# Optimization experiments

Measured on AMD Instinct MI355X. Metric: run time of the kernel, lower is better.

Reference implementation:

```python
import jax, jax.numpy as jnp
import numpy as np

N = 8192      # atoms
B = 64        # molecules
E = 262144    # edges
S = 4         # species
NMAX = 8      # radial basis size
CUT = 5.0     # cutoff radius
AVG_ATOMS = 128.0
E_SCALE = 1.0
PS_DIM = (S * NMAX) ** 2 * 4  # l_max=3 -> 4 l channels -> 4096
H1, H2 = 1024, 1024
OUT = 1


def _sph_harm(u):
    # real spherical harmonics up to l=3, input unit vectors [E,3] -> [E,16]
    x, y, z = u[:, 0], u[:, 1], u[:, 2]
    x2, y2, z2 = x * x, y * y, z * z
    return jnp.stack([
        0.28209479 * jnp.ones_like(x),
        0.48860251 * y, 0.48860251 * z, 0.48860251 * x,
        1.09254843 * x * y, 1.09254843 * y * z, 0.31539157 * (3.0 * z2 - 1.0),
        1.09254843 * x * z, 0.54627422 * (x2 - y2),
        0.59004359 * y * (3.0 * x2 - y2), 2.89061144 * x * y * z,
        0.45704579 * y * (5.0 * z2 - 1.0), 0.37317633 * z * (5.0 * z2 - 3.0),
        0.45704579 * x * (5.0 * z2 - 1.0), 1.44530572 * z * (x2 - y2),
        0.59004359 * x * (x2 - 3.0 * y2),
    ], axis=-1)


def setup_inputs() -> dict:
    key = jax.random.key(0)
    ks = jax.random.split(key, 12)
    positions = jax.random.normal(ks[0], (N, 3), dtype=jnp.float32) * 1.5  # dense cloud so many pairs < CUT
    cells = jnp.tile(20.0 * jnp.eye(3, dtype=jnp.float32)[None], (B, 1, 1))
    numbers = jax.random.randint(ks[1], (N,), 0, S)
    edge_indices = jax.random.randint(ks[2], (2, E), 0, N)
    edge_offsets = jnp.zeros((E, 3), dtype=jnp.float32)
    batch = jnp.arange(N) // (N // B)
    gamma = 1.0 + 0.1 * jax.random.normal(ks[3], (PS_DIM,), dtype=jnp.float32)
    beta = 0.1 * jax.random.normal(ks[4], (PS_DIM,), dtype=jnp.float32)
    W_ps = jax.random.normal(ks[5], (PS_DIM, OUT), dtype=jnp.float32) / np.sqrt(PS_DIM)
    W1 = jax.random.normal(ks[6], (PS_DIM, H1), dtype=jnp.float32) / np.sqrt(PS_DIM)
    W2 = jax.random.normal(ks[7], (H1, H2), dtype=jnp.float32) / np.sqrt(H1)
    W3 = jax.random.normal(ks[8], (H2, OUT), dtype=jnp.float32) / np.sqrt(H2)
    W_comp = jax.random.normal(ks[9], (S, OUT), dtype=jnp.float32) / np.sqrt(S)
    return dict(positions=positions, cells=cells, numbers=numbers,
                edge_indices=edge_indices, edge_offsets=edge_offsets, batch=batch,
                gamma=gamma, beta=beta, W_ps=W_ps, W1=W1, W2=W2, W3=W3, W_comp=W_comp)


def reference(positions, cells, numbers, edge_indices, edge_offsets, batch,
              gamma, beta, W_ps, W1, W2, W3, W_comp):
    i, j = edge_indices[0], edge_indices[1]  # center, neighbor
    # periodic shift: fractional offsets through the cell of the center's molecule
    shift = jnp.einsum('ec,ecd->ed', edge_offsets, cells[batch[i]])
    rvec = positions[j] - positions[i] + shift                      # [E,3]
    r = jnp.sqrt(jnp.sum(rvec * rvec, axis=-1) + 1e-12)             # [E]
    u = rvec / r[:, None]
    fc = 0.5 * (jnp.cos(jnp.pi * jnp.minimum(r, CUT) / CUT) + 1.0) * (r < CUT)
    n = jnp.arange(1, NMAX + 1, dtype=positions.dtype)
    R = fc[:, None] * jnp.sin(jnp.pi * n[None, :] * r[:, None] / CUT) / r[:, None]  # [E,NMAX]
    Y = _sph_harm(u)                                                # [E,16]
    edge_feat = R[:, :, None] * Y[:, None, :]                       # [E,NMAX,16]
    # spherical expansion c[i, species(j), n, lm] via scatter-add
    seg = i * S + numbers[j]
    c = jax.ops.segment_sum(edge_feat, seg, num_segments=N * S)     # [N*S,NMAX,16]
    c = c.reshape(N, S * NMAX, 16)
    # power spectrum: contract over m within each l block
    bounds = [(0, 1), (1, 4), (4, 9), (9, 16)]
    p = [jnp.einsum('ixm,iym->ixy', c[:, :, s:e], c[:, :, s:e]) for s, e in bounds]
    ps = jnp.stack(p, axis=-1).reshape(N, PS_DIM)                   # [N,4096]
    # LayerNorm (eps=1e-5, affine)
    mu = jnp.mean(ps, axis=-1, keepdims=True)
    var = jnp.var(ps, axis=-1, keepdims=True)
    psn = (ps - mu) / jnp.sqrt(var + 1e-5) * gamma + beta
    # linear branch + MLP branch
    psl = psn @ W_ps                                                # [N,1]
    h = jax.nn.silu(psn @ W1)
    h = jax.nn.silu(h @ W2)
    psnn = h @ W3                                                   # [N,1]
    # pool atomic energies into per-molecule totals (index_add)
    energies = jax.ops.segment_sum(psl + psnn, batch, num_segments=B) / AVG_ATOMS
    # eval path: composition baseline
    comp = jax.ops.segment_sum(jax.nn.one_hot(numbers, S, dtype=psn.dtype), batch, num_segments=B)
    return energies * E_SCALE + comp @ W_comp                       # [B,1]
```

## Files before the change

kernel.cpp:

```cpp
#include <hip/hip_runtime.h>
#include <hip/hip_bf16.h>
#include <math.h>

#define N_ATOMS 8192
#define B_BATCH 64
#define E_EDGES 262144
#define S_SPEC 4
#define NMAX 8
#define PS_DIM 4096
#define H1_DIM 1024
#define CAP4 48
#define CUTR 5.0f
#define PI_F 3.14159265358979f

typedef __bf16 bf16;
typedef bf16 bf16x8 __attribute__((ext_vector_type(8)));
typedef float floatx4 __attribute__((ext_vector_type(4)));
typedef int intx8 __attribute__((ext_vector_type(8)));
typedef unsigned char u8;

__device__ __forceinline__ void g2lds16(const void* g, void* l) {
    __builtin_amdgcn_global_load_lds(
        (const __attribute__((address_space(1))) void*)g,
        (__attribute__((address_space(3))) void*)l, 16, 0, 0);
}

__device__ __forceinline__ int pk_fp8x4(float a, float b, float c, float d) {
    int lo = __builtin_amdgcn_cvt_pk_fp8_f32(a, b, 0, false);
    return __builtin_amdgcn_cvt_pk_fp8_f32(c, d, lo, true);
}

__global__ __launch_bounds__(256) void scatter_kernel(
    const float* __restrict__ pos, const float* __restrict__ cells,
    const int* __restrict__ numbers, const int* __restrict__ ei,
    const float* __restrict__ eo, const int* __restrict__ batch,
    int* __restrict__ cnt, float4* __restrict__ bucket)
{
    int e = blockIdx.x * 256 + threadIdx.x;
    int i = ei[e];
    int j = ei[E_EDGES + e];
    int b = batch[i];
    const float* cell = cells + b * 9;
    float o0 = eo[e * 3 + 0], o1 = eo[e * 3 + 1], o2 = eo[e * 3 + 2];
    float rv[3];
    #pragma unroll
    for (int d = 0; d < 3; ++d) {
        float shift = o0 * cell[0 * 3 + d] + o1 * cell[1 * 3 + d] + o2 * cell[2 * 3 + d];
        rv[d] = pos[j * 3 + d] - pos[i * 3 + d] + shift;
    }
    float r2 = rv[0] * rv[0] + rv[1] * rv[1] + rv[2] * rv[2] + 1e-12f;
    if (r2 >= CUTR * CUTR) return;
    float r = sqrtf(r2);
    float a1 = r * (PI_F / CUTR);
    int sp = numbers[j];
    int q = i * S_SPEC + sp;
    int slot = atomicAdd(&cnt[q], 1);
    if (slot < CAP4)
        bucket[q * CAP4 + slot] = make_float4(rv[0], rv[1], rv[2], a1);
}

__global__ __launch_bounds__(256) void accum_ps_kernel(
    const float4* __restrict__ bucket, const int* __restrict__ cnt,
    const float* __restrict__ gamma, const float* __restrict__ beta,
    const float* __restrict__ Wps, u8* __restrict__ psn, float* __restrict__ psl)
{
    __shared__ __align__(16) float cl[4][32 * 20];
    __shared__ __align__(16) u8 ps_s8[PS_DIM];
    __shared__ float red[8];
    __shared__ float red2[4];

    int t = threadIdx.x;
    int wv = t >> 6, lane = t & 63;
    int atom0 = blockIdx.x * 4;

    {
        int atom = atom0 + wv;
        int sp_l = lane >> 4;
        int nidx = (lane >> 1) & 7;
        float nf = (float)(nidx + 1);
        int par = lane & 1;

        int myCnt = cnt[atom * S_SPEC + sp_l];
        if (myCnt > CAP4) myCnt = CAP4;
        int m1 = max(myCnt, __shfl_xor(myCnt, 16));
        int mx = max(m1, __shfl_xor(m1, 32));

        const float4* q = bucket + (size_t)(atom * S_SPEC + sp_l) * CAP4;
        float acc[8] = {};
        #pragma unroll 2
        for (int e = 0; e < mx; ++e) {
            float4 d = q[e];
            bool valid = e < myCnt;
            float a1 = d.w;
            float inv_r = (PI_F / CUTR) * __frcp_rn(a1);
            float fc = 0.5f * __cosf(a1) + 0.5f;
            float rn = fc * inv_r * __sinf(nf * a1);
            rn = valid ? rn : 0.0f;

            float x = d.x * inv_r, y = d.y * inv_r, z = d.z * inv_r;
            float x2 = x * x, y2 = y * y, z2 = z * z;
            float Ys[8];
            if (par == 0) {
                Ys[0] = 0.28209479f;
                Ys[1] = 0.48860251f * y;
                Ys[2] = 0.48860251f * z;
                Ys[3] = 0.48860251f * x;
                Ys[4] = 1.09254843f * x * y;
                Ys[5] = 1.09254843f * y * z;
                Ys[6] = 0.31539157f * (3.0f * z2 - 1.0f);
                Ys[7] = 1.09254843f * x * z;
            } else {
                Ys[0] = 0.54627422f * (x2 - y2);
                Ys[1] = 0.59004359f * y * (3.0f * x2 - y2);
                Ys[2] = 2.89061144f * x * y * z;
                Ys[3] = 0.45704579f * y * (5.0f * z2 - 1.0f);
                Ys[4] = 0.37317633f * z * (5.0f * z2 - 3.0f);
                Ys[5] = 0.45704579f * x * (5.0f * z2 - 1.0f);
                Ys[6] = 1.44530572f * z * (x2 - y2);
                Ys[7] = 0.59004359f * x * (x2 - 3.0f * y2);
            }
            #pragma unroll
            for (int k = 0; k < 8; ++k) acc[k] += rn * Ys[k];
        }
        int X = sp_l * 8 + nidx;
        float* dst = &cl[wv][X * 20 + par * 8];
        *(float4*)(dst + 0) = make_float4(acc[0], acc[1], acc[2], acc[3]);
        *(float4*)(dst + 4) = make_float4(acc[4], acc[5], acc[6], acc[7]);
    }
    __syncthreads();

    for (int a = 0; a < 4; ++a) {
        int atom = atom0 + a;
        const float* cl_x = cl[a];

        int y = t & 31;
        int xb = t >> 5;
        float4 cya = *(const float4*)&cl_x[y * 20 + 0];
        float4 cyb = *(const float4*)&cl_x[y * 20 + 4];
        float4 cyc = *(const float4*)&cl_x[y * 20 + 8];
        float4 cyd = *(const float4*)&cl_x[y * 20 + 12];

        float ps[4][4];
        float sum = 0.0f, sumsq = 0.0f;
        #pragma unroll
        for (int q = 0; q < 4; ++q) {
            int x = xb + 8 * q;
            float4 xa = *(const float4*)&cl_x[x * 20 + 0];
            float4 xbv = *(const float4*)&cl_x[x * 20 + 4];
            float4 xc = *(const float4*)&cl_x[x * 20 + 8];
            float4 xd = *(const float4*)&cl_x[x * 20 + 12];
            float s0 = xa.x * cya.x;
            float s1 = xa.y * cya.y + xa.z * cya.z + xa.w * cya.w;
            float s2 = xbv.x * cyb.x + xbv.y * cyb.y + xbv.z * cyb.z + xbv.w * cyb.w
                     + xc.x * cyc.x;
            float s3 = xc.y * cyc.y + xc.z * cyc.z + xc.w * cyc.w
                     + xd.x * cyd.x + xd.y * cyd.y + xd.z * cyd.z + xd.w * cyd.w;
            ps[q][0] = s0; ps[q][1] = s1; ps[q][2] = s2; ps[q][3] = s3;
            sum += s0 + s1 + s2 + s3;
            sumsq += s0 * s0 + s1 * s1 + s2 * s2 + s3 * s3;
        }
        #pragma unroll
        for (int o = 32; o > 0; o >>= 1) {
            sum += __shfl_down(sum, o);
            sumsq += __shfl_down(sumsq, o);
        }
        if ((t & 63) == 0) { red[wv] = sum; red[4 + wv] = sumsq; }
        __syncthreads();
        float tot = red[0] + red[1] + red[2] + red[3];
        float totsq = red[4] + red[5] + red[6] + red[7];
        float mu = tot * (1.0f / PS_DIM);
        float var = totsq * (1.0f / PS_DIM) - mu * mu;
        float inv = rsqrtf(var + 1e-5f);

        float pacc = 0.0f;
        #pragma unroll
        for (int q = 0; q < 4; ++q) {
            int p = t + 256 * q;
            float4 g = *(const float4*)(gamma + p * 4);
            float4 bt = *(const float4*)(beta + p * 4);
            float4 w = *(const float4*)(Wps + p * 4);
            float v0 = (ps[q][0] - mu) * inv * g.x + bt.x;
            float v1 = (ps[q][1] - mu) * inv * g.y + bt.y;
            float v2 = (ps[q][2] - mu) * inv * g.z + bt.z;
            float v3 = (ps[q][3] - mu) * inv * g.w + bt.w;
            pacc += v0 * w.x + v1 * w.y + v2 * w.z + v3 * w.w;
            ((int*)ps_s8)[p] = pk_fp8x4(v0, v1, v2, v3);
        }
        __syncthreads();
        u8* rowp = psn + (size_t)atom * PS_DIM;
        int key = atom & 7;
        int gcs = (t & ~7) | ((t & 7) ^ key);
        *(uint4*)(rowp + (size_t)gcs * 16) = *(const uint4*)(ps_s8 + (size_t)t * 16);

        #pragma unroll
        for (int o = 32; o > 0; o >>= 1) pacc += __shfl_down(pacc, o);
        if ((t & 63) == 0) red2[wv] = pacc;
        __syncthreads();
        if (t == 0) psl[atom] = red2[0] + red2[1] + red2[2] + red2[3];
    }
}

__global__ __launch_bounds__(256) void transpose_convert2(
    const float* __restrict__ W1, u8* __restrict__ Wt1,
    const float* __restrict__ W2, u8* __restrict__ Wt2)
{
    const float* W; u8* Wt; int K; float scale; int bx;
    if (blockIdx.x < 128) { W = W1; Wt = Wt1; K = PS_DIM; scale = 64.0f; bx = blockIdx.x; }
    else                  { W = W2; Wt = Wt2; K = H1_DIM; scale = 32.0f; bx = blockIdx.x - 128; }
    const int Nc = H1_DIM;
    __shared__ float t[32][33];
    int k0 = bx * 32, n0 = blockIdx.y * 32;
    int tx = threadIdx.x & 31, ty = threadIdx.x >> 5;
    #pragma unroll
    for (int r = 0; r < 32; r += 8)
        t[ty + r][tx] = W[(size_t)(k0 + ty + r) * Nc + n0 + tx];
    __syncthreads();
    if (threadIdx.x < 64) {
        int nl = threadIdx.x >> 1, cc = threadIdx.x & 1;
        int n = n0 + nl;
        unsigned int w[4];
        #pragma unroll
        for (int g = 0; g < 4; ++g) {
            int kb = cc * 16 + g * 4;
            w[g] = (unsigned int)pk_fp8x4(
                t[kb + 0][nl] * scale, t[kb + 1][nl] * scale,
                t[kb + 2][nl] * scale, t[kb + 3][nl] * scale);
        }
        int gc = (k0 >> 4) + cc;
        int gcs = (gc & ~7) | ((gc & 7) ^ (n & 7));
        *(uint4*)(Wt + (size_t)n * K + (size_t)gcs * 16) = make_uint4(w[0], w[1], w[2], w[3]);
    }
}

template<int OUT_FP8>
__global__ __launch_bounds__(256) void gemm_f8_kernel(
    const u8* __restrict__ A, const u8* __restrict__ Bt,
    void* __restrict__ H, int M, int Nc, int K, float invs)
{
    __shared__ __align__(16) char smem[24576];
    int tid = threadIdx.x;
    int bm = blockIdx.x, bn = blockIdx.y;
    int wave = tid >> 6, lane = tid & 63;
    int wm = (wave >> 1) * 32, wn = (wave & 1) * 64;
    int lm = lane & 15, quad = lane >> 4;

    floatx4 acc[2][4] = {};
    const int rowA0 = bm * 64, rowB0 = bn * 128;
    const size_t stride = (size_t)K;
    const char* Ab = (const char*)A + (size_t)rowA0 * stride;
    const char* Bb = (const char*)Bt + (size_t)rowB0 * stride;
    const int sA = 0x7F7F7F7F, sB = 0x7F7F7F7F;

    for (int k0 = 0; k0 < K; k0 += 128) {
        #pragma unroll
        for (int s = 0; s < 2; ++s) {
            int L = s * 256 + tid;
            int row = L >> 3, boff = (L & 7) * 16;
            int lbase = (s * 256 + wave * 64) * 16;
            g2lds16(Ab + (size_t)row * stride + k0 + boff, smem + lbase);
        }
        #pragma unroll
        for (int s = 0; s < 4; ++s) {
            int L = s * 256 + tid;
            int row = L >> 3, boff = (L & 7) * 16;
            int lbase = (s * 256 + wave * 64) * 16;
            g2lds16(Bb + (size_t)row * stride + k0 + boff, smem + 8192 + lbase);
        }
        __syncthreads();
        int key = lm & 7;
        int c0 = (2 * quad) ^ key, c1 = (2 * quad + 1) ^ key;
        intx8 af[2], bfr[4];
        #pragma unroll
        for (int mi = 0; mi < 2; ++mi) {
            const char* base = smem + (wm + mi * 16 + lm) * 128;
            uint4 lo = *(const uint4*)(base + c0 * 16);
            uint4 hi = *(const uint4*)(base + c1 * 16);
            af[mi][0] = lo.x; af[mi][1] = lo.y; af[mi][2] = lo.z; af[mi][3] = lo.w;
            af[mi][4] = hi.x; af[mi][5] = hi.y; af[mi][6] = hi.z; af[mi][7] = hi.w;
        }
        #pragma unroll
        for (int ni = 0; ni < 4; ++ni) {
            const char* base = smem + 8192 + (wn + ni * 16 + lm) * 128;
            uint4 lo = *(const uint4*)(base + c0 * 16);
            uint4 hi = *(const uint4*)(base + c1 * 16);
            bfr[ni][0] = lo.x; bfr[ni][1] = lo.y; bfr[ni][2] = lo.z; bfr[ni][3] = lo.w;
            bfr[ni][4] = hi.x; bfr[ni][5] = hi.y; bfr[ni][6] = hi.z; bfr[ni][7] = hi.w;
        }
        #pragma unroll
        for (int mi = 0; mi < 2; ++mi)
            #pragma unroll
            for (int ni = 0; ni < 4; ++ni)
                acc[mi][ni] = __builtin_amdgcn_mfma_scale_f32_16x16x128_f8f6f4(
                    af[mi], bfr[ni], acc[mi][ni], 0, 0, 0, sA, 0, sB);
        __syncthreads();
    }

    if (OUT_FP8) {
        u8* Cs8 = (u8*)smem;
        #pragma unroll
        for (int mi = 0; mi < 2; ++mi)
            #pragma unroll
            for (int ni = 0; ni < 4; ++ni)
                #pragma unroll
                for (int r = 0; r < 4; ++r) {
                    int row = wm + mi * 16 + quad * 4 + r;
                    int col = wn + ni * 16 + lm;
                    float v = acc[mi][ni][r] * invs;
                    v = v / (1.0f + __expf(-v));
                    int pk = __builtin_amdgcn_cvt_pk_fp8_f32(v, 0.0f, 0, false);
                    Cs8[row * 128 + col] = (u8)(pk & 0xFF);
                }
        __syncthreads();
        #pragma unroll
        for (int c2 = 0; c2 < 2; ++c2) {
            int L = c2 * 256 + tid;
            int row = L >> 3, cc = L & 7;
            int gcs = cc ^ (row & 7);
            *(uint4*)((u8*)H + (size_t)(rowA0 + row) * Nc + (size_t)(bn * 8 + gcs) * 16) =
                *(const uint4*)(Cs8 + (size_t)L * 16);
        }
    } else {
        bf16* Cs = (bf16*)smem;
        #pragma unroll
        for (int mi = 0; mi < 2; ++mi)
            #pragma unroll
            for (int ni = 0; ni < 4; ++ni)
                #pragma unroll
                for (int r = 0; r < 4; ++r) {
                    int row = wm + mi * 16 + quad * 4 + r;
                    int col = wn + ni * 16 + lm;
                    float v = acc[mi][ni][r] * invs;
                    v = v / (1.0f + __expf(-v));
                    Cs[row * 128 + col] = (bf16)v;
                }
        __syncthreads();
        const size_t strideH = (size_t)Nc * 2;
        #pragma unroll
        for (int c2 = 0; c2 < 4; ++c2) {
            int L = c2 * 256 + tid;
            int row = L >> 4, cc = L & 15;
            *(uint4*)((char*)H + (size_t)(rowA0 + row) * strideH + (size_t)(bn * 16 + cc) * 16) =
                *(const uint4*)((char*)Cs + (size_t)L * 16);
        }
    }
}

__global__ __launch_bounds__(256) void tail_kernel(
    const bf16* __restrict__ h2, const float* __restrict__ W3,
    const float* __restrict__ psl, const int* __restrict__ numbers,
    const float* __restrict__ Wcomp, float* __restrict__ out)
{
    int b = blockIdx.x;
    int t = threadIdx.x;
    int wv = t >> 6, lane = t & 63;
    __shared__ float tot;
    __shared__ int cnt4[S_SPEC];
    if (t == 0) tot = 0.0f;
    if (t < S_SPEC) cnt4[t] = 0;
    __syncthreads();

    if (t < 128) {
        int a = b * 128 + t;
        atomicAdd(&tot, psl[a]);
        atomicAdd(&cnt4[numbers[a]], 1);
    }

    float acc = 0.0f;
    for (int k = 0; k < 32; ++k) {
        int atom = b * 128 + wv * 32 + k;
        const bf16* h = h2 + (size_t)atom * H1_DIM;
        #pragma unroll
        for (int q2 = 0; q2 < 2; ++q2) {
            int k0 = (lane + 64 * q2) * 8;
            bf16x8 hv = *(const bf16x8*)(h + k0);
            float4 w0 = *(const float4*)(W3 + k0);
            float4 w1 = *(const float4*)(W3 + k0 + 4);
            acc += (float)hv[0] * w0.x + (float)hv[1] * w0.y
                 + (float)hv[2] * w0.z + (float)hv[3] * w0.w
                 + (float)hv[4] * w1.x + (float)hv[5] * w1.y
                 + (float)hv[6] * w1.z + (float)hv[7] * w1.w;
        }
    }
    #pragma unroll
    for (int o = 32; o > 0; o >>= 1) acc += __shfl_down(acc, o);
    if (lane == 0) atomicAdd(&tot, acc);
    __syncthreads();
    if (t == 0) {
        float r = tot * (1.0f / 128.0f);
        #pragma unroll
        for (int s = 0; s < S_SPEC; ++s) r += (float)cnt4[s] * Wcomp[s];
        out[b] = r;
    }
}

extern "C" void kernel_launch(void* const* d_in, const int* in_sizes, int n_in,
                              void* d_out, int out_size, void* d_ws, size_t ws_size,
                              hipStream_t stream)
{
    const float* positions = (const float*)d_in[0];
    const float* cells     = (const float*)d_in[1];
    const int*   numbers   = (const int*)d_in[2];
    const int*   ei        = (const int*)d_in[3];
    const float* eo        = (const float*)d_in[4];
    const int*   batch     = (const int*)d_in[5];
    const float* gamma     = (const float*)d_in[6];
    const float* beta      = (const float*)d_in[7];
    const float* W_ps      = (const float*)d_in[8];
    const float* W1        = (const float*)d_in[9];
    const float* W2        = (const float*)d_in[10];
    const float* W3        = (const float*)d_in[11];
    const float* W_comp    = (const float*)d_in[12];
    float* out = (float*)d_out;

    char* ws = (char*)d_ws;
    float4* bucket = (float4*)ws;  ws += (size_t)N_ATOMS * S_SPEC * CAP4 * 16;
    u8*    psn  = (u8*)ws;     ws += (size_t)N_ATOMS * PS_DIM;
    u8*    h1   = (u8*)ws;     ws += (size_t)N_ATOMS * H1_DIM;
    bf16*  h2   = (bf16*)ws;   ws += (size_t)N_ATOMS * H1_DIM * 2;
    u8*    Wt1  = (u8*)ws;     ws += (size_t)H1_DIM * PS_DIM;
    u8*    Wt2  = (u8*)ws;     ws += (size_t)H1_DIM * H1_DIM;
    float* psl  = (float*)ws;  ws += (size_t)N_ATOMS * 4;
    int*   cnt  = (int*)ws;    ws += (size_t)N_ATOMS * S_SPEC * 4;

    hipMemsetAsync(cnt, 0, N_ATOMS * S_SPEC * sizeof(int), stream);

    scatter_kernel<<<E_EDGES / 256, 256, 0, stream>>>(
        positions, cells, numbers, ei, eo, batch, cnt, bucket);

    transpose_convert2<<<dim3(160, 32), 256, 0, stream>>>(W1, Wt1, W2, Wt2);

    accum_ps_kernel<<<N_ATOMS / 4, 256, 0, stream>>>(
        bucket, cnt, gamma, beta, W_ps, psn, psl);

    gemm_f8_kernel<1><<<dim3(N_ATOMS / 64, H1_DIM / 128), 256, 0, stream>>>(
        psn, Wt1, (void*)h1, N_ATOMS, H1_DIM, PS_DIM, 1.0f / 64.0f);
    gemm_f8_kernel<0><<<dim3(N_ATOMS / 64, H1_DIM / 128), 256, 0, stream>>>(
        h1, Wt2, (void*)h2, N_ATOMS, H1_DIM, H1_DIM, 1.0f / 32.0f);

    tail_kernel<<<B_BATCH, 256, 0, stream>>>(h2, W3, psl, numbers, W_comp, out);
}
```

Before: 214.0 us.

## Fuse W3 projection into second GEMM epilogue and merge scatter with weight transpose

The second MLP GEMM no longer writes the bf16 h2 activation matrix. Its epilogue applies SiLU, dots each tile with W3 and atomically adds the partial into a per-molecule accumulator. This removes a 16MB write and re-read plus the heavy tail kernel. The edge scatter and the weight transpose/convert are merged into one launch, and the memset is widened to clear the new accumulator. In exchange, float atomics make the summation order nondeterministic.

Result: slower. 225.8 us (+5.5%).

```diff
diff --git a/kernel.cpp b/kernel.cpp
--- a/kernel.cpp
+++ b/kernel.cpp
@@ -30,33 +30,67 @@
     return __builtin_amdgcn_cvt_pk_fp8_f32(c, d, lo, true);
 }
 
-__global__ __launch_bounds__(256) void scatter_kernel(
+__global__ __launch_bounds__(256) void scatter_trans_kernel(
     const float* __restrict__ pos, const float* __restrict__ cells,
     const int* __restrict__ numbers, const int* __restrict__ ei,
     const float* __restrict__ eo, const int* __restrict__ batch,
-    int* __restrict__ cnt, float4* __restrict__ bucket)
-{
-    int e = blockIdx.x * 256 + threadIdx.x;
-    int i = ei[e];
-    int j = ei[E_EDGES + e];
-    int b = batch[i];
-    const float* cell = cells + b * 9;
-    float o0 = eo[e * 3 + 0], o1 = eo[e * 3 + 1], o2 = eo[e * 3 + 2];
-    float rv[3];
-    #pragma unroll
-    for (int d = 0; d < 3; ++d) {
-        float shift = o0 * cell[0 * 3 + d] + o1 * cell[1 * 3 + d] + o2 * cell[2 * 3 + d];
-        rv[d] = pos[j * 3 + d] - pos[i * 3 + d] + shift;
-    }
-    float r2 = rv[0] * rv[0] + rv[1] * rv[1] + rv[2] * rv[2] + 1e-12f;
-    if (r2 >= CUTR * CUTR) return;
-    float r = sqrtf(r2);
-    float a1 = r * (PI_F / CUTR);
-    int sp = numbers[j];
-    int q = i * S_SPEC + sp;
-    int slot = atomicAdd(&cnt[q], 1);
-    if (slot < CAP4)
-        bucket[q * CAP4 + slot] = make_float4(rv[0], rv[1], rv[2], a1);
+    int* __restrict__ cnt, float4* __restrict__ bucket,
+    const float* __restrict__ W1, u8* __restrict__ Wt1,
+    const float* __restrict__ W2, u8* __restrict__ Wt2)
+{
+    __shared__ float t[32][33];
+    if (blockIdx.x < E_EDGES / 256) {
+        int e = blockIdx.x * 256 + threadIdx.x;
+        int i = ei[e];
+        int j = ei[E_EDGES + e];
+        int b = batch[i];
+        const float* cell = cells + b * 9;
+        float o0 = eo[e * 3 + 0], o1 = eo[e * 3 + 1], o2 = eo[e * 3 + 2];
+        float rv[3];
+        #pragma unroll
+        for (int d = 0; d < 3; ++d) {
+            float shift = o0 * cell[0 * 3 + d] + o1 * cell[1 * 3 + d] + o2 * cell[2 * 3 + d];
+            rv[d] = pos[j * 3 + d] - pos[i * 3 + d] + shift;
+        }
+        float r2 = rv[0] * rv[0] + rv[1] * rv[1] + rv[2] * rv[2] + 1e-12f;
+        if (r2 >= CUTR * CUTR) return;
+        float r = sqrtf(r2);
+        float a1 = r * (PI_F / CUTR);
+        int sp = numbers[j];
+        int q = i * S_SPEC + sp;
+        int slot = atomicAdd(&cnt[q], 1);
+        if (slot < CAP4)
+            bucket[q * CAP4 + slot] = make_float4(rv[0], rv[1], rv[2], a1);
+    } else {
+        int bid = blockIdx.x - E_EDGES / 256;
+        int bx = bid >> 5;
+        int by = bid & 31;
+        const float* W; u8* Wt; int K; float scale;
+        if (bx < 128) { W = W1; Wt = Wt1; K = PS_DIM; scale = 64.0f; }
+        else          { W = W2; Wt = Wt2; K = H1_DIM; scale = 32.0f; bx -= 128; }
+        const int Nc = H1_DIM;
+        int k0 = bx * 32, n0 = by * 32;
+        int tx = threadIdx.x & 31, ty = threadIdx.x >> 5;
+        #pragma unroll
+        for (int r = 0; r < 32; r += 8)
+            t[ty + r][tx] = W[(size_t)(k0 + ty + r) * Nc + n0 + tx];
+        __syncthreads();
+        if (threadIdx.x < 64) {
+            int nl = threadIdx.x >> 1, cc = threadIdx.x & 1;
+            int n = n0 + nl;
+            unsigned int w[4];
+            #pragma unroll
+            for (int g = 0; g < 4; ++g) {
+                int kb = cc * 16 + g * 4;
+                w[g] = (unsigned int)pk_fp8x4(
+                    t[kb + 0][nl] * scale, t[kb + 1][nl] * scale,
+                    t[kb + 2][nl] * scale, t[kb + 3][nl] * scale);
+            }
+            int gc = (k0 >> 4) + cc;
+            int gcs = (gc & ~7) | ((gc & 7) ^ (n & 7));
+            *(uint4*)(Wt + (size_t)n * K + (size_t)gcs * 16) = make_uint4(w[0], w[1], w[2], w[3]);
+        }
+    }
 }
 
 __global__ __launch_bounds__(256) void accum_ps_kernel(
@@ -200,42 +234,9 @@
     }
 }
 
-__global__ __launch_bounds__(256) void transpose_convert2(
-    const float* __restrict__ W1, u8* __restrict__ Wt1,
-    const float* __restrict__ W2, u8* __restrict__ Wt2)
-{
-    const float* W; u8* Wt; int K; float scale; int bx;
-    if (blockIdx.x < 128) { W = W1; Wt = Wt1; K = PS_DIM; scale = 64.0f; bx = blockIdx.x; }
-    else                  { W = W2; Wt = Wt2; K = H1_DIM; scale = 32.0f; bx = blockIdx.x - 128; }
-    const int Nc = H1_DIM;
-    __shared__ float t[32][33];
-    int k0 = bx * 32, n0 = blockIdx.y * 32;
-    int tx = threadIdx.x & 31, ty = threadIdx.x >> 5;
-    #pragma unroll
-    for (int r = 0; r < 32; r += 8)
-        t[ty + r][tx] = W[(size_t)(k0 + ty + r) * Nc + n0 + tx];
-    __syncthreads();
-    if (threadIdx.x < 64) {
-        int nl = threadIdx.x >> 1, cc = threadIdx.x & 1;
-        int n = n0 + nl;
-        unsigned int w[4];
-        #pragma unroll
-        for (int g = 0; g < 4; ++g) {
-            int kb = cc * 16 + g * 4;
-            w[g] = (unsigned int)pk_fp8x4(
-                t[kb + 0][nl] * scale, t[kb + 1][nl] * scale,
-                t[kb + 2][nl] * scale, t[kb + 3][nl] * scale);
-        }
-        int gc = (k0 >> 4) + cc;
-        int gcs = (gc & ~7) | ((gc & 7) ^ (n & 7));
-        *(uint4*)(Wt + (size_t)n * K + (size_t)gcs * 16) = make_uint4(w[0], w[1], w[2], w[3]);
-    }
-}
-
-template<int OUT_FP8>
 __global__ __launch_bounds__(256) void gemm_f8_kernel(
     const u8* __restrict__ A, const u8* __restrict__ Bt,
-    void* __restrict__ H, int M, int Nc, int K, float invs)
+    u8* __restrict__ H, int M, int Nc, int K, float invs)
 {
     __shared__ __align__(16) char smem[24576];
     int tid = threadIdx.x;
@@ -295,98 +296,131 @@
         __syncthreads();
     }
 
-    if (OUT_FP8) {
-        u8* Cs8 = (u8*)smem;
+    u8* Cs8 = (u8*)smem;
+    #pragma unroll
+    for (int mi = 0; mi < 2; ++mi)
+        #pragma unroll
+        for (int ni = 0; ni < 4; ++ni)
+            #pragma unroll
+            for (int r = 0; r < 4; ++r) {
+                int row = wm + mi * 16 + quad * 4 + r;
+                int col = wn + ni * 16 + lm;
+                float v = acc[mi][ni][r] * invs;
+                v = v / (1.0f + __expf(-v));
+                int pk = __builtin_amdgcn_cvt_pk_fp8_f32(v, 0.0f, 0, false);
+                Cs8[row * 128 + col] = (u8)(pk & 0xFF);
+            }
+    __syncthreads();
+    #pragma unroll
+    for (int c2 = 0; c2 < 2; ++c2) {
+        int L = c2 * 256 + tid;
+        int row = L >> 3, cc = L & 7;
+        int gcs = cc ^ (row & 7);
+        *(uint4*)(H + (size_t)(rowA0 + row) * Nc + (size_t)(bn * 8 + gcs) * 16) =
+            *(const uint4*)(Cs8 + (size_t)L * 16);
+    }
+}
+
+__global__ __launch_bounds__(256) void gemm2_fused_kernel(
+    const u8* __restrict__ A, const u8* __restrict__ Bt,
+    const float* __restrict__ W3, float* __restrict__ nn_batch,
+    int Nc, int K, float invs)
+{
+    __shared__ __align__(16) char smem[24576];
+    int tid = threadIdx.x;
+    int bm = blockIdx.x, bn = blockIdx.y;
+    int wave = tid >> 6, lane = tid & 63;
+    int wm = (wave >> 1) * 32, wn = (wave & 1) * 64;
+    int lm = lane & 15, quad = lane >> 4;
+
+    floatx4 acc[2][4] = {};
+    const int rowA0 = bm * 64, rowB0 = bn * 128;
+    const size_t stride = (size_t)K;
+    const char* Ab = (const char*)A + (size_t)rowA0 * stride;
+    const char* Bb = (const char*)Bt + (size_t)rowB0 * stride;
+    const int sA = 0x7F7F7F7F, sB = 0x7F7F7F7F;
+
+    for (int k0 = 0; k0 < K; k0 += 128) {
+        #pragma unroll
+        for (int s = 0; s < 2; ++s) {
+            int L = s * 256 + tid;
+            int row = L >> 3, boff = (L & 7) * 16;
+            int lbase = (s * 256 + wave * 64) * 16;
+            g2lds16(Ab + (size_t)row * stride + k0 + boff, smem + lbase);
+        }
+        #pragma unroll
+        for (int s = 0; s < 4; ++s) {
+            int L = s * 256 + tid;
+            int row = L >> 3, boff = (L & 7) * 16;
+            int lbase = (s * 256 + wave * 64) * 16;
+            g2lds16(Bb + (size_t)row * stride + k0 + boff, smem + 8192 + lbase);
+        }
+        __syncthreads();
+        int key = lm & 7;
+        int c0 = (2 * quad) ^ key, c1 = (2 * quad + 1) ^ key;
+        intx8 af[2], bfr[4];
+        #pragma unroll
+        for (int mi = 0; mi < 2; ++mi) {
+            const char* base = smem + (wm + mi * 16 + lm) * 128;
+            uint4 lo = *(const uint4*)(base + c0 * 16);
+            uint4 hi = *(const uint4*)(base + c1 * 16);
+            af[mi][0] = lo.x; af[mi][1] = lo.y; af[mi][2] = lo.z; af[mi][3] = lo.w;
+            af[mi][4] = hi.x; af[mi][5] = hi.y; af[mi][6] = hi.z; af[mi][7] = hi.w;
+        }
+        #pragma unroll
+        for (int ni = 0; ni < 4; ++ni) {
+            const char* base = smem + 8192 + (wn + ni * 16 + lm) * 128;
+            uint4 lo = *(const uint4*)(base + c0 * 16);
+            uint4 hi = *(const uint4*)(base + c1 * 16);
+            bfr[ni][0] = lo.x; bfr[ni][1] = lo.y; bfr[ni][2] = lo.z; bfr[ni][3] = lo.w;
+            bfr[ni][4] = hi.x; bfr[ni][5] = hi.y; bfr[ni][6] = hi.z; bfr[ni][7] = hi.w;
+        }
         #pragma unroll
         for (int mi = 0; mi < 2; ++mi)
             #pragma unroll
             for (int ni = 0; ni < 4; ++ni)
-                #pragma unroll
-                for (int r = 0; r < 4; ++r) {
-                    int row = wm + mi * 16 + quad * 4 + r;
-                    int col = wn + ni * 16 + lm;
-                    float v = acc[mi][ni][r] * invs;
-                    v = v / (1.0f + __expf(-v));
-                    int pk = __builtin_amdgcn_cvt_pk_fp8_f32(v, 0.0f, 0, false);
-                    Cs8[row * 128 + col] = (u8)(pk & 0xFF);
-                }
-        __syncthreads();
-        #pragma unroll
-        for (int c2 = 0; c2 < 2; ++c2) {
-            int L = c2 * 256 + tid;
-            int row = L >> 3, cc = L & 7;
-            int gcs = cc ^ (row & 7);
-            *(uint4*)((u8*)H + (size_t)(rowA0 + row) * Nc + (size_t)(bn * 8 + gcs) * 16) =
-                *(const uint4*)(Cs8 + (size_t)L * 16);
-        }
-    } else {
-        bf16* Cs = (bf16*)smem;
+                acc[mi][ni] = __builtin_amdgcn_mfma_scale_f32_16x16x128_f8f6f4(
+                    af[mi], bfr[ni], acc[mi][ni], 0, 0, 0, sA, 0, sB);
+        __syncthreads();
+    }
+
+    float lt = 0.0f;
+    #pragma unroll
+    for (int ni = 0; ni < 4; ++ni) {
+        float w3v = W3[bn * 128 + wn + ni * 16 + lm];
         #pragma unroll
         for (int mi = 0; mi < 2; ++mi)
             #pragma unroll
-            for (int ni = 0; ni < 4; ++ni)
-                #pragma unroll
-                for (int r = 0; r < 4; ++r) {
-                    int row = wm + mi * 16 + quad * 4 + r;
-                    int col = wn + ni * 16 + lm;
-                    float v = acc[mi][ni][r] * invs;
-                    v = v / (1.0f + __expf(-v));
-                    Cs[row * 128 + col] = (bf16)v;
-                }
-        __syncthreads();
-        const size_t strideH = (size_t)Nc * 2;
-        #pragma unroll
-        for (int c2 = 0; c2 < 4; ++c2) {
-            int L = c2 * 256 + tid;
-            int row = L >> 4, cc = L & 15;
-            *(uint4*)((char*)H + (size_t)(rowA0 + row) * strideH + (size_t)(bn * 16 + cc) * 16) =
-                *(const uint4*)((char*)Cs + (size_t)L * 16);
-        }
-    }
-}
-
-__global__ __launch_bounds__(256) void tail_kernel(
-    const bf16* __restrict__ h2, const float* __restrict__ W3,
+            for (int r = 0; r < 4; ++r) {
+                float v = acc[mi][ni][r] * invs;
+                v = v / (1.0f + __expf(-v));
+                lt += v * w3v;
+            }
+    }
+    #pragma unroll
+    for (int o = 32; o > 0; o >>= 1) lt += __shfl_down(lt, o);
+    if (lane == 0) atomicAdd(&nn_batch[bm >> 1], lt);
+}
+
+__global__ __launch_bounds__(128) void finalize_kernel(
     const float* __restrict__ psl, const int* __restrict__ numbers,
-    const float* __restrict__ Wcomp, float* __restrict__ out)
-{
-    int b = blockIdx.x;
-    int t = threadIdx.x;
-    int wv = t >> 6, lane = t & 63;
-    __shared__ float tot;
+    const float* __restrict__ nn_batch, const float* __restrict__ Wcomp,
+    float* __restrict__ out)
+{
+    int b = blockIdx.x, t = threadIdx.x;
+    __shared__ float sh[2];
     __shared__ int cnt4[S_SPEC];
-    if (t == 0) tot = 0.0f;
     if (t < S_SPEC) cnt4[t] = 0;
     __syncthreads();
-
-    if (t < 128) {
-        int a = b * 128 + t;
-        atomicAdd(&tot, psl[a]);
-        atomicAdd(&cnt4[numbers[a]], 1);
-    }
-
-    float acc = 0.0f;
-    for (int k = 0; k < 32; ++k) {
-        int atom = b * 128 + wv * 32 + k;
-        const bf16* h = h2 + (size_t)atom * H1_DIM;
-        #pragma unroll
-        for (int q2 = 0; q2 < 2; ++q2) {
-            int k0 = (lane + 64 * q2) * 8;
-            bf16x8 hv = *(const bf16x8*)(h + k0);
-            float4 w0 = *(const float4*)(W3 + k0);
-            float4 w1 = *(const float4*)(W3 + k0 + 4);
-            acc += (float)hv[0] * w0.x + (float)hv[1] * w0.y
-                 + (float)hv[2] * w0.z + (float)hv[3] * w0.w
-                 + (float)hv[4] * w1.x + (float)hv[5] * w1.y
-                 + (float)hv[6] * w1.z + (float)hv[7] * w1.w;
-        }
-    }
+    int a = b * 128 + t;
+    float e = psl[a];
+    atomicAdd(&cnt4[numbers[a]], 1);
     #pragma unroll
-    for (int o = 32; o > 0; o >>= 1) acc += __shfl_down(acc, o);
-    if (lane == 0) atomicAdd(&tot, acc);
+    for (int o = 32; o > 0; o >>= 1) e += __shfl_down(e, o);
+    if ((t & 63) == 0) sh[t >> 6] = e;
     __syncthreads();
     if (t == 0) {
-        float r = tot * (1.0f / 128.0f);
+        float r = (sh[0] + sh[1] + nn_batch[b]) * (1.0f / 128.0f);
         #pragma unroll
         for (int s = 0; s < S_SPEC; ++s) r += (float)cnt4[s] * Wcomp[s];
         out[b] = r;
@@ -416,26 +450,24 @@
     float4* bucket = (float4*)ws;  ws += (size_t)N_ATOMS * S_SPEC * CAP4 * 16;
     u8*    psn  = (u8*)ws;     ws += (size_t)N_ATOMS * PS_DIM;
     u8*    h1   = (u8*)ws;     ws += (size_t)N_ATOMS * H1_DIM;
-    bf16*  h2   = (bf16*)ws;   ws += (size_t)N_ATOMS * H1_DIM * 2;
     u8*    Wt1  = (u8*)ws;     ws += (size_t)H1_DIM * PS_DIM;
     u8*    Wt2  = (u8*)ws;     ws += (size_t)H1_DIM * H1_DIM;
     float* psl  = (float*)ws;  ws += (size_t)N_ATOMS * 4;
     int*   cnt  = (int*)ws;    ws += (size_t)N_ATOMS * S_SPEC * 4;
-
-    hipMemsetAsync(cnt, 0, N_ATOMS * S_SPEC * sizeof(int), stream);
-
-    scatter_kernel<<<E_EDGES / 256, 256, 0, stream>>>(
-        positions, cells, numbers, ei, eo, batch, cnt, bucket);
-
-    transpose_convert2<<<dim3(160, 32), 256, 0, stream>>>(W1, Wt1, W2, Wt2);
+    float* nn_batch = (float*)ws; ws += (size_t)B_BATCH * 4;
+
+    hipMemsetAsync(cnt, 0, N_ATOMS * S_SPEC * sizeof(int) + B_BATCH * sizeof(float), stream);
+
+    scatter_trans_kernel<<<E_EDGES / 256 + 160 * 32, 256, 0, stream>>>(
+        positions, cells, numbers, ei, eo, batch, cnt, bucket, W1, Wt1, W2, Wt2);
 
     accum_ps_kernel<<<N_ATOMS / 4, 256, 0, stream>>>(
         bucket, cnt, gamma, beta, W_ps, psn, psl);
 
-    gemm_f8_kernel<1><<<dim3(N_ATOMS / 64, H1_DIM / 128), 256, 0, stream>>>(
-        psn, Wt1, (void*)h1, N_ATOMS, H1_DIM, PS_DIM, 1.0f / 64.0f);
-    gemm_f8_kernel<0><<<dim3(N_ATOMS / 64, H1_DIM / 128), 256, 0, stream>>>(
-        h1, Wt2, (void*)h2, N_ATOMS, H1_DIM, H1_DIM, 1.0f / 32.0f);
-
-    tail_kernel<<<B_BATCH, 256, 0, stream>>>(h2, W3, psl, numbers, W_comp, out);
-}
+    gemm_f8_kernel<<<dim3(N_ATOMS / 64, H1_DIM / 128), 256, 0, stream>>>(
+        psn, Wt1, h1, N_ATOMS, H1_DIM, PS_DIM, 1.0f / 64.0f);
+    gemm2_fused_kernel<<<dim3(N_ATOMS / 64, H1_DIM / 128), 256, 0, stream>>>(
+        h1, Wt2, W3, nn_batch, H1_DIM, H1_DIM, 1.0f / 32.0f);
+
+    finalize_kernel<<<B_BATCH, 128, 0, stream>>>(psl, numbers, nn_batch, W_comp, out);
+}
```
